# Kernel optimization log

Measured on AMD Instinct MI355X. Metric: run time of the kernel, lower is better.

The kernel has to match this reference:

```python
import jax, jax.numpy as jnp
import numpy as np

N_NODES = 100000
N_EDGES = 3200000
OUT_FEATURES = 16


def setup_inputs() -> dict:
    key = jax.random.key(0)
    k1, k2 = jax.random.split(key)
    edge = jax.random.randint(k1, (2, N_EDGES), 0, N_NODES, dtype=jnp.int64 if jax.config.jax_enable_x64 else jnp.int32)
    edge_w = jax.random.normal(k2, (N_EDGES, OUT_FEATURES), dtype=jnp.float32)
    return {
        "edge": edge,
        "edge_w": edge_w,
        "N": N_NODES,
        "E": N_EDGES,
        "out_features": OUT_FEATURES,
    }


def reference(edge, edge_w, N, E, out_features):
    # torch.sparse.sum over dim=1 of a [N, N, F] COO tensor == segment-sum of
    # edge_w grouped by the source index edge[0], producing dense [N, F].
    src = edge[0]  # [E]
    out = jax.ops.segment_sum(edge_w, src, num_segments=N)  # [N, F]
    return out
```

## Files before the change

### kernel.cpp

```cpp
#include <hip/hip_runtime.h>
#include <hip/hip_cooperative_groups.h>
#include <math.h>

namespace cg = cooperative_groups;


#define F 16
#define NPB 1024
#define NPB_SHIFT 10
#define MAXB 128
#define SCALE 256.0f
#define INV_SCALE (1.0f / 256.0f)

#define NBIN 256
#define BINT 512
#define NSPLIT 8
#define SLICES (NBIN / NSPLIT)
#define ACCT 512

#define FB 1024
#define FT 512
#define NBIN2 1024
#define NSPLIT2 8
#define SLICES2 (NBIN2 / NSPLIT2)

__device__ __forceinline__ unsigned long long qpack(float4 v) {
    long long q0 = (long long)__float2int_rn(v.x * SCALE);
    long long q1 = (long long)__float2int_rn(v.y * SCALE);
    long long q2 = (long long)__float2int_rn(v.z * SCALE);
    long long q3 = (long long)__float2int_rn(v.w * SCALE);
    return (unsigned long long)((q3 << 48) + (q2 << 32) + (q1 << 16) + q0);
}

__global__ __launch_bounds__(FT, 8) void spmm_fused(
    const int* __restrict__ src,
    const float* __restrict__ w,
    unsigned int* __restrict__ idbuf,
    unsigned int* __restrict__ cnt,
    unsigned long long* __restrict__ pbuf,
    float* __restrict__ out,
    int E, int B, int capb, int per_block, int N)
{
    __shared__ unsigned long long acc[NPB * 4];
    __shared__ unsigned int pos[MAXB];
    __shared__ unsigned int ksh[SLICES2];

    cg::grid_group grid = cg::this_grid();
    const int tid = threadIdx.x;
    const int bid = blockIdx.x;
    const int n4  = N * 4;
    unsigned long long* spill = pbuf + (size_t)NSPLIT2 * (size_t)n4;

    for (int i = tid; i < B; i += FT) pos[i] = 0;
    __syncthreads();

    const int lo = bid * per_block;
    const int hi = min(E, lo + per_block);
    for (int e = lo + tid * 2; e < hi; e += FT * 2) {
        int sa, sb = -1;
        if (e + 1 < hi) { int2 s2 = *(const int2*)(src + e); sa = s2.x; sb = s2.y; }
        else            { sa = src[e]; }
        {
            const int bk = sa >> NPB_SHIFT;
            const unsigned int off = (unsigned int)(sa & (NPB - 1));
            const unsigned int r = atomicAdd(&pos[bk], 1u);
            if (r < (unsigned int)capb) {
                idbuf[((size_t)bid * B + bk) * capb + r] = (off << 22) | (unsigned int)e;
            } else {
                const float4* wr = (const float4*)(w + (size_t)e * F);
                #pragma unroll
                for (int qq = 0; qq < 4; ++qq)
                    atomicAdd(&spill[(size_t)sa * 4 + qq], qpack(wr[qq]));
            }
        }
        if (sb >= 0) {
            const int e1 = e + 1;
            const int bk = sb >> NPB_SHIFT;
            const unsigned int off = (unsigned int)(sb & (NPB - 1));
            const unsigned int r = atomicAdd(&pos[bk], 1u);
            if (r < (unsigned int)capb) {
                idbuf[((size_t)bid * B + bk) * capb + r] = (off << 22) | (unsigned int)e1;
            } else {
                const float4* wr = (const float4*)(w + (size_t)e1 * F);
                #pragma unroll
                for (int qq = 0; qq < 4; ++qq)
                    atomicAdd(&spill[(size_t)sb * 4 + qq], qpack(wr[qq]));
            }
        }
    }
    __syncthreads();
    for (int i = tid; i < B; i += FT)
        cnt[bid * B + i] = min(pos[i], (unsigned int)capb);

    __threadfence();
    grid.sync();

    const int q   = tid & 3;
    const int st  = tid >> 2;
    const int sg  = st >> 4;
    const int s16 = st & 15;

    for (int t = bid; t < B * NSPLIT2; t += FB) {
        const int b  = t >> 3;
        const int sp = t & 7;

        for (int i = tid; i < NPB * 4; i += FT) acc[i] = 0ULL;
        if (tid < SLICES2) ksh[tid] = cnt[(sp * SLICES2 + tid) * B + b];
        __syncthreads();

        for (int sr = 0; sr < 16; ++sr) {
            const int s   = sr * 8 + sg;
            const int blk = sp * SLICES2 + s;
            const unsigned int k = ksh[s];
            const unsigned int* cell = idbuf + ((size_t)blk * B + b) * capb;
            #pragma unroll
            for (int tr = 0; tr < 4; ++tr) {
                const unsigned int slot = (unsigned int)(tr * 16 + s16);
                if (slot < k) {
                    const unsigned int entry = cell[slot];
                    const unsigned int off = entry >> 22;
                    const unsigned int e   = entry & 0x3FFFFFu;
                    const float4 v = *(const float4*)(w + (size_t)e * F + q * 4);
                    atomicAdd(&acc[off * 4 + q], qpack(v));
                }
            }
        }
        {
            const int s = st;
            const unsigned int k = ksh[s];
            if (k > 64u) {
                const int blk = sp * SLICES2 + s;
                const unsigned int* cell = idbuf + ((size_t)blk * B + b) * capb;
                for (unsigned int i = 64u; i < k; ++i) {
                    const unsigned int entry = cell[i];
                    const unsigned int off = entry >> 22;
                    const unsigned int e   = entry & 0x3FFFFFu;
                    const float4 v = *(const float4*)(w + (size_t)e * F + q * 4);
                    atomicAdd(&acc[off * 4 + q], qpack(v));
                }
            }
        }
        __syncthreads();

        const int nbase = b << NPB_SHIFT;
        const int lim = min(NPB, N - nbase);
        unsigned long long* dst = pbuf + (size_t)sp * n4 + (size_t)nbase * 4;
        for (int i = tid; i < lim * 4; i += FT) dst[i] = acc[i];
        __syncthreads();
    }

    __threadfence();
    grid.sync();

    for (int idx = bid * FT + tid; idx < n4; idx += FB * FT) {
        unsigned long long a = 0;
        #pragma unroll
        for (int s = 0; s < NSPLIT2 + 1; ++s) a += pbuf[(size_t)s * n4 + idx];
        long long tt = (long long)a;
        const int s0 = (int)(short)(tt & 0xffff);  tt = (tt - s0) >> 16;
        const int s1 = (int)(short)(tt & 0xffff);  tt = (tt - s1) >> 16;
        const int s2 = (int)(short)(tt & 0xffff);  tt = (tt - s2) >> 16;
        const int s3 = (int)(short)(tt & 0xffff);
        float4 o;
        o.x = (float)s0 * INV_SCALE;
        o.y = (float)s1 * INV_SCALE;
        o.z = (float)s2 * INV_SCALE;
        o.w = (float)s3 * INV_SCALE;
        ((float4*)out)[idx] = o;
    }
}

__global__ __launch_bounds__(BINT) void spmm_bin_id(
    const int* __restrict__ src,
    const float* __restrict__ w,
    unsigned int* __restrict__ idbuf,
    unsigned int* __restrict__ cnt,
    unsigned long long* __restrict__ spill,
    int E, int B, int capb, int per_block)
{
    __shared__ unsigned int pos[MAXB];
    const int tid = threadIdx.x;
    for (int i = tid; i < B; i += BINT) pos[i] = 0;
    __syncthreads();

    const int lo = blockIdx.x * per_block;
    const int hi = min(E, lo + per_block);

    for (int e = lo + tid; e < hi; e += BINT) {
        const int s = src[e];
        const int bk = s >> NPB_SHIFT;
        const unsigned int off = (unsigned int)(s & (NPB - 1));
        const unsigned int r = atomicAdd(&pos[bk], 1u);
        if (r < (unsigned int)capb) {
            idbuf[((size_t)blockIdx.x * B + bk) * capb + r] =
                (off << 22) | (unsigned int)e;
        } else {
            const float4* wr = (const float4*)(w + (size_t)e * F);
            #pragma unroll
            for (int q = 0; q < 4; ++q)
                atomicAdd(&spill[(size_t)s * 4 + q], qpack(wr[q]));
        }
    }
    __syncthreads();
    for (int i = tid; i < B; i += BINT)
        cnt[blockIdx.x * B + i] = min(pos[i], (unsigned int)capb);
}

__global__ __launch_bounds__(ACCT) void spmm_acc_g(
    const float* __restrict__ w,
    const unsigned int* __restrict__ idbuf,
    const unsigned int* __restrict__ cnt,
    unsigned long long* __restrict__ pbuf,
    int B, int capb, int N)
{
    __shared__ unsigned long long acc[NPB * 4];
    const int tid = threadIdx.x;
    const int b  = blockIdx.x >> 3;
    const int sp = blockIdx.x & 7;

    for (int i = tid; i < NPB * 4; i += ACCT) acc[i] = 0ULL;
    __syncthreads();

    const int q  = tid & 3;
    const int ei = tid >> 2;

    for (int sl = 0; sl < SLICES; ++sl) {
        const int blk = sp * SLICES + sl;
        const unsigned int k = cnt[blk * B + b];
        const unsigned int* base = idbuf + ((size_t)blk * B + b) * capb;
        for (unsigned int i = ei; i < k; i += ACCT / 4) {
            const unsigned int entry = base[i];
            const unsigned int off = entry >> 22;
            const unsigned int e   = entry & 0x3FFFFFu;
            const float4 v = *(const float4*)(w + (size_t)e * F + q * 4);
            atomicAdd(&acc[off * 4 + q], qpack(v));
        }
    }
    __syncthreads();

    const int nbase = b << NPB_SHIFT;
    const int lim = min(NPB, N - nbase);
    unsigned long long* dst = pbuf + (size_t)sp * ((size_t)N * 4) + (size_t)nbase * 4;
    for (int i = tid; i < lim * 4; i += ACCT) dst[i] = acc[i];
}

__global__ __launch_bounds__(256) void spmm_decode9(
    const unsigned long long* __restrict__ pbuf,
    float* __restrict__ out, int n4)
{
    const int idx = blockIdx.x * 256 + threadIdx.x;
    if (idx >= n4) return;
    unsigned long long a = 0;
    #pragma unroll
    for (int s = 0; s < NSPLIT + 1; ++s) a += pbuf[(size_t)s * n4 + idx];

    long long t = (long long)a;
    const int s0 = (int)(short)(t & 0xffff);  t = (t - s0) >> 16;
    const int s1 = (int)(short)(t & 0xffff);  t = (t - s1) >> 16;
    const int s2 = (int)(short)(t & 0xffff);  t = (t - s2) >> 16;
    const int s3 = (int)(short)(t & 0xffff);

    float4 o;
    o.x = (float)s0 * INV_SCALE;
    o.y = (float)s1 * INV_SCALE;
    o.z = (float)s2 * INV_SCALE;
    o.w = (float)s3 * INV_SCALE;
    ((float4*)out)[idx] = o;
}

__global__ __launch_bounds__(256) void spmm_scatter_gs(
    const int* __restrict__ src,
    const float* __restrict__ w,
    unsigned long long* __restrict__ ws,
    int total)
{
    const int stride = gridDim.x * blockDim.x;
    for (int idx = blockIdx.x * blockDim.x + threadIdx.x; idx < total; idx += stride) {
        const int e = idx >> 2, lane = idx & 3;
        const float4 v = ((const float4*)w)[idx];
        atomicAdd(&ws[src[e] * 4 + lane], qpack(v));
    }
}

__global__ __launch_bounds__(256) void spmm_decode1(
    const unsigned long long* __restrict__ ws,
    float* __restrict__ out, int n4)
{
    const int idx = blockIdx.x * 256 + threadIdx.x;
    if (idx >= n4) return;
    long long t = (long long)ws[idx];
    const int s0 = (int)(short)(t & 0xffff);  t = (t - s0) >> 16;
    const int s1 = (int)(short)(t & 0xffff);  t = (t - s1) >> 16;
    const int s2 = (int)(short)(t & 0xffff);  t = (t - s2) >> 16;
    const int s3 = (int)(short)(t & 0xffff);
    float4 o;
    o.x = (float)s0 * INV_SCALE;
    o.y = (float)s1 * INV_SCALE;
    o.z = (float)s2 * INV_SCALE;
    o.w = (float)s3 * INV_SCALE;
    ((float4*)out)[idx] = o;
}

extern "C" void kernel_launch(void* const* d_in, const int* in_sizes, int n_in,
                              void* d_out, int out_size, void* d_ws, size_t ws_size,
                              hipStream_t stream) {
    const int* edge = (const int*)d_in[0];
    const float* ew = (const float*)d_in[1];
    const int E = in_sizes[0] / 2;
    const int N = out_size / F;
    const int n4 = N * 4;
    float* out = (float*)d_out;

    const int B = (N + NPB - 1) >> NPB_SHIFT;

    static int coop_state = -1;
    if (coop_state < 0) {
        int maxb = 0, cus = 0;
        hipDeviceProp_t prop;
        int dev = 0;
        hipError_t e1 = hipGetDevice(&dev);
        hipError_t e2 = hipGetDeviceProperties(&prop, dev);
        if (e2 == hipSuccess) cus = prop.multiProcessorCount;
        hipError_t e3 = hipOccupancyMaxActiveBlocksPerMultiprocessor(
            &maxb, spmm_fused, FT, 0);
        coop_state = (e1 == hipSuccess && e3 == hipSuccess &&
                      (long)maxb * (long)cus >= FB) ? 1 : 0;
    }

    const double mean2 = (double)E / ((double)NBIN2 * (double)B);
    const double sig2  = sqrt(mean2 > 1.0 ? mean2 : 1.0);
    int capb2 = (int)(mean2 + 6.0 * sig2 + 8.0);
    capb2 = (capb2 + 15) & ~15;
    const size_t cnt2_b  = (size_t)NBIN2 * B * 4;
    const size_t pbuf2_b = (size_t)(NSPLIT2 + 1) * n4 * 8;
    const size_t fixed2  = ((cnt2_b + 255) & ~(size_t)255) + pbuf2_b + 512;
    if (ws_size > fixed2) {
        const size_t idroom = ws_size - fixed2;
        int capb2_max = (int)(idroom / ((size_t)NBIN2 * B * 4));
        capb2_max &= ~15;
        if (capb2 > capb2_max) capb2 = capb2_max;
    }
    const int capb2_min = ((int)(mean2 + 3.0 * sig2) + 15) & ~15;
    const size_t idbuf2_b = (size_t)NBIN2 * B * capb2 * 4;
    size_t off_cnt2  = (idbuf2_b + 255) & ~(size_t)255;
    size_t off_pbuf2 = (off_cnt2 + cnt2_b + 255) & ~(size_t)255;
    const size_t need2 = off_pbuf2 + pbuf2_b;

    const double mean = (double)E / ((double)NBIN * (double)B);
    int capb = (int)(mean + 8.0 * sqrt(mean > 1.0 ? mean : 1.0) + 16.0);
    capb = (capb + 15) & ~15;
    const size_t idbuf_b = (size_t)NBIN * B * capb * 4;
    size_t off_cnt  = (idbuf_b + 255) & ~(size_t)255;
    const size_t cnt_b = (size_t)NBIN * B * 4;
    size_t off_pbuf = (off_cnt + cnt_b + 255) & ~(size_t)255;
    const size_t pbuf_b = (size_t)(NSPLIT + 1) * n4 * 8;
    const size_t need = off_pbuf + pbuf_b;

    const int block = 256;
    const bool shape_ok = (B <= MAXB) && (E > 0) && (E < (1 << 22));

    if (shape_ok && coop_state == 1 && capb2 >= capb2_min && capb2 >= 16 &&
        need2 <= ws_size) {
        unsigned int* idbuf = (unsigned int*)d_ws;
        unsigned int* cnt   = (unsigned int*)((char*)d_ws + off_cnt2);
        unsigned long long* pbuf = (unsigned long long*)((char*)d_ws + off_pbuf2);
        unsigned long long* spill = pbuf + (size_t)NSPLIT2 * n4;

        hipMemsetAsync(spill, 0, (size_t)n4 * 8, stream);

        int per_block2 = (E + FB - 1) / FB;
        per_block2 = (per_block2 + 1) & ~1;

        int E_ = E, B_ = B, N_ = N, cap_ = capb2, pb_ = per_block2;
        void* kargs[] = { (void*)&edge, (void*)&ew, (void*)&idbuf, (void*)&cnt,
                          (void*)&pbuf, (void*)&out,
                          (void*)&E_, (void*)&B_, (void*)&cap_, (void*)&pb_, (void*)&N_ };
        hipError_t lr = hipLaunchCooperativeKernel(
            spmm_fused, dim3(FB), dim3(FT), kargs, 0, stream);
        if (lr == hipSuccess) return;
        coop_state = 0;
    }

    if (shape_ok && need <= ws_size) {
        unsigned int* idbuf = (unsigned int*)d_ws;
        unsigned int* cnt   = (unsigned int*)((char*)d_ws + off_cnt);
        unsigned long long* pbuf  = (unsigned long long*)((char*)d_ws + off_pbuf);
        unsigned long long* spill = pbuf + (size_t)NSPLIT * n4;

        hipMemsetAsync(spill, 0, (size_t)n4 * 8, stream);

        const int per_block = (E + NBIN - 1) / NBIN;
        spmm_bin_id<<<NBIN, BINT, 0, stream>>>(edge, ew, idbuf, cnt, spill,
                                               E, B, capb, per_block);
        spmm_acc_g<<<B * NSPLIT, ACCT, 0, stream>>>(ew, idbuf, cnt, pbuf,
                                                    B, capb, N);
        spmm_decode9<<<(n4 + block - 1) / block, block, 0, stream>>>(pbuf, out, n4);
    } else {
        unsigned long long* ws = (unsigned long long*)d_ws;
        hipMemsetAsync(ws, 0, (size_t)n4 * 8, stream);
        spmm_scatter_gs<<<2048, block, 0, stream>>>(edge, ew, ws, E * 4);
        spmm_decode1<<<(n4 + block - 1) / block, block, 0, stream>>>(ws, out, n4);
    }
}
```

Baseline: 355.2 us.

## Stage quantized edge payloads in bins instead of edge ids to avoid gather

The binning phase now reads each edge's 16 weights once, quantizes them, and writes the 32-byte packed payload plus a 16-bit node offset into the bin slot, instead of writing a packed (offset, edge id) word. The accumulate phase then streams these payloads contiguously with one lane per slot, and the shared accumulator moves to a feature-major layout, rather than gathering weight rows by edge id. This removes the random gather of the weight array in phase two. In exchange it adds much more workspace traffic (34 bytes per slot versus 4), lowers the occupancy hint in launch bounds, and shrinks the capacity cap, which may push more edges onto the global atomic spill path.

```diff
diff --git a/kernel.cpp b/kernel.cpp
--- a/kernel.cpp
+++ b/kernel.cpp
@@ -32,10 +32,11 @@
     return (unsigned long long)((q3 << 48) + (q2 << 32) + (q1 << 16) + q0);
 }
 
-__global__ __launch_bounds__(FT, 8) void spmm_fused(
+__global__ __launch_bounds__(FT, 4) void spmm_fused(
     const int* __restrict__ src,
     const float* __restrict__ w,
-    unsigned int* __restrict__ idbuf,
+    unsigned long long* __restrict__ pay,
+    unsigned short* __restrict__ off16,
     unsigned int* __restrict__ cnt,
     unsigned long long* __restrict__ pbuf,
     float* __restrict__ out,
@@ -56,37 +57,40 @@
 
     const int lo = bid * per_block;
     const int hi = min(E, lo + per_block);
-    for (int e = lo + tid * 2; e < hi; e += FT * 2) {
+    for (int e0 = lo + tid * 2; e0 < hi; e0 += FT * 2) {
         int sa, sb = -1;
-        if (e + 1 < hi) { int2 s2 = *(const int2*)(src + e); sa = s2.x; sb = s2.y; }
-        else            { sa = src[e]; }
-        {
-            const int bk = sa >> NPB_SHIFT;
-            const unsigned int off = (unsigned int)(sa & (NPB - 1));
+        if (e0 + 1 < hi) { int2 s2 = *(const int2*)(src + e0); sa = s2.x; sb = s2.y; }
+        else             { sa = src[e0]; }
+        #pragma unroll
+        for (int u = 0; u < 2; ++u) {
+            const int s = (u == 0) ? sa : sb;
+            if (s < 0 && u == 1) break;
+            const int e = e0 + u;
+            const float4* wr = (const float4*)(w + (size_t)e * F);
+            const float4 w0 = wr[0], w1 = wr[1], w2 = wr[2], w3 = wr[3];
+            const unsigned long long q0 = qpack(w0);
+            const unsigned long long q1 = qpack(w1);
+            const unsigned long long q2 = qpack(w2);
+            const unsigned long long q3 = qpack(w3);
+
+            const int bk = s >> NPB_SHIFT;
+            const unsigned int off = (unsigned int)(s & (NPB - 1));
             const unsigned int r = atomicAdd(&pos[bk], 1u);
             if (r < (unsigned int)capb) {
-                idbuf[((size_t)bid * B + bk) * capb + r] = (off << 22) | (unsigned int)e;
+                const size_t slot = ((size_t)bid * B + bk) * capb + r;
+                ulonglong2* ps = (ulonglong2*)(pay + slot * 4);
+                ulonglong2 p0; p0.x = q0; p0.y = q1;
+                ulonglong2 p1; p1.x = q2; p1.y = q3;
+                ps[0] = p0;
+                ps[1] = p1;
+                off16[slot] = (unsigned short)off;
             } else {
-                const float4* wr = (const float4*)(w + (size_t)e * F);
-                #pragma unroll
-                for (int qq = 0; qq < 4; ++qq)
-                    atomicAdd(&spill[(size_t)sa * 4 + qq], qpack(wr[qq]));
+                atomicAdd(&spill[(size_t)s * 4 + 0], q0);
+                atomicAdd(&spill[(size_t)s * 4 + 1], q1);
+                atomicAdd(&spill[(size_t)s * 4 + 2], q2);
+                atomicAdd(&spill[(size_t)s * 4 + 3], q3);
             }
         }
-        if (sb >= 0) {
-            const int e1 = e + 1;
-            const int bk = sb >> NPB_SHIFT;
-            const unsigned int off = (unsigned int)(sb & (NPB - 1));
-            const unsigned int r = atomicAdd(&pos[bk], 1u);
-            if (r < (unsigned int)capb) {
-                idbuf[((size_t)bid * B + bk) * capb + r] = (off << 22) | (unsigned int)e1;
-            } else {
-                const float4* wr = (const float4*)(w + (size_t)e1 * F);
-                #pragma unroll
-                for (int qq = 0; qq < 4; ++qq)
-                    atomicAdd(&spill[(size_t)sb * 4 + qq], qpack(wr[qq]));
-            }
-        }
     }
     __syncthreads();
     for (int i = tid; i < B; i += FT)
@@ -95,10 +99,8 @@
     __threadfence();
     grid.sync();
 
-    const int q   = tid & 3;
-    const int st  = tid >> 2;
-    const int sg  = st >> 4;
-    const int s16 = st & 15;
+    const int wv = tid >> 6;
+    const int ln = tid & 63;
 
     for (int t = bid; t < B * NSPLIT2; t += FB) {
         const int b  = t >> 3;
@@ -108,36 +110,19 @@
         if (tid < SLICES2) ksh[tid] = cnt[(sp * SLICES2 + tid) * B + b];
         __syncthreads();
 
-        for (int sr = 0; sr < 16; ++sr) {
-            const int s   = sr * 8 + sg;
-            const int blk = sp * SLICES2 + s;
+        for (int s = wv; s < SLICES2; s += 8) {
             const unsigned int k = ksh[s];
-            const unsigned int* cell = idbuf + ((size_t)blk * B + b) * capb;
-            #pragma unroll
-            for (int tr = 0; tr < 4; ++tr) {
-                const unsigned int slot = (unsigned int)(tr * 16 + s16);
-                if (slot < k) {
-                    const unsigned int entry = cell[slot];
-                    const unsigned int off = entry >> 22;
-                    const unsigned int e   = entry & 0x3FFFFFu;
-                    const float4 v = *(const float4*)(w + (size_t)e * F + q * 4);
-                    atomicAdd(&acc[off * 4 + q], qpack(v));
-                }
-            }
-        }
-        {
-            const int s = st;
-            const unsigned int k = ksh[s];
-            if (k > 64u) {
-                const int blk = sp * SLICES2 + s;
-                const unsigned int* cell = idbuf + ((size_t)blk * B + b) * capb;
-                for (unsigned int i = 64u; i < k; ++i) {
-                    const unsigned int entry = cell[i];
-                    const unsigned int off = entry >> 22;
-                    const unsigned int e   = entry & 0x3FFFFFu;
-                    const float4 v = *(const float4*)(w + (size_t)e * F + q * 4);
-                    atomicAdd(&acc[off * 4 + q], qpack(v));
-                }
+            const size_t cell = (size_t)(sp * SLICES2 + s) * B + b;
+            const ulonglong2* pp = (const ulonglong2*)(pay + cell * capb * 4);
+            const unsigned short* oo = off16 + cell * capb;
+            for (unsigned int slot = (unsigned int)ln; slot < k; slot += 64u) {
+                const ulonglong2 p0 = pp[slot * 2 + 0];
+                const ulonglong2 p1 = pp[slot * 2 + 1];
+                const unsigned int off = oo[slot];
+                atomicAdd(&acc[0 * NPB + off], p0.x);
+                atomicAdd(&acc[1 * NPB + off], p0.y);
+                atomicAdd(&acc[2 * NPB + off], p1.x);
+                atomicAdd(&acc[3 * NPB + off], p1.y);
             }
         }
         __syncthreads();
@@ -145,7 +130,8 @@
         const int nbase = b << NPB_SHIFT;
         const int lim = min(NPB, N - nbase);
         unsigned long long* dst = pbuf + (size_t)sp * n4 + (size_t)nbase * 4;
-        for (int i = tid; i < lim * 4; i += FT) dst[i] = acc[i];
+        for (int i = tid; i < lim * 4; i += FT)
+            dst[i] = acc[(i & 3) * NPB + (i >> 2)];
         __syncthreads();
     }
 
@@ -331,18 +317,21 @@
     const double sig2  = sqrt(mean2 > 1.0 ? mean2 : 1.0);
     int capb2 = (int)(mean2 + 6.0 * sig2 + 8.0);
     capb2 = (capb2 + 15) & ~15;
-    const size_t cnt2_b  = (size_t)NBIN2 * B * 4;
+    const size_t cells   = (size_t)NBIN2 * B;
+    const size_t cnt2_b  = cells * 4;
     const size_t pbuf2_b = (size_t)(NSPLIT2 + 1) * n4 * 8;
-    const size_t fixed2  = ((cnt2_b + 255) & ~(size_t)255) + pbuf2_b + 512;
+    const size_t fixed2  = ((cnt2_b + 255) & ~(size_t)255) + pbuf2_b + 1024;
     if (ws_size > fixed2) {
-        const size_t idroom = ws_size - fixed2;
-        int capb2_max = (int)(idroom / ((size_t)NBIN2 * B * 4));
+        const size_t room = ws_size - fixed2;
+        int capb2_max = (int)(room / (cells * 34));
         capb2_max &= ~15;
         if (capb2 > capb2_max) capb2 = capb2_max;
     }
     const int capb2_min = ((int)(mean2 + 3.0 * sig2) + 15) & ~15;
-    const size_t idbuf2_b = (size_t)NBIN2 * B * capb2 * 4;
-    size_t off_cnt2  = (idbuf2_b + 255) & ~(size_t)255;
+    const size_t pay_b   = cells * (size_t)capb2 * 32;
+    size_t off_off16 = (pay_b + 255) & ~(size_t)255;
+    const size_t off16_b = cells * (size_t)capb2 * 2;
+    size_t off_cnt2  = (off_off16 + off16_b + 255) & ~(size_t)255;
     size_t off_pbuf2 = (off_cnt2 + cnt2_b + 255) & ~(size_t)255;
     const size_t need2 = off_pbuf2 + pbuf2_b;
 
@@ -361,8 +350,9 @@
 
     if (shape_ok && coop_state == 1 && capb2 >= capb2_min && capb2 >= 16 &&
         need2 <= ws_size) {
-        unsigned int* idbuf = (unsigned int*)d_ws;
-        unsigned int* cnt   = (unsigned int*)((char*)d_ws + off_cnt2);
+        unsigned long long* pay = (unsigned long long*)d_ws;
+        unsigned short* off16   = (unsigned short*)((char*)d_ws + off_off16);
+        unsigned int* cnt       = (unsigned int*)((char*)d_ws + off_cnt2);
         unsigned long long* pbuf = (unsigned long long*)((char*)d_ws + off_pbuf2);
         unsigned long long* spill = pbuf + (size_t)NSPLIT2 * n4;
 
@@ -372,8 +362,8 @@
         per_block2 = (per_block2 + 1) & ~1;
 
         int E_ = E, B_ = B, N_ = N, cap_ = capb2, pb_ = per_block2;
-        void* kargs[] = { (void*)&edge, (void*)&ew, (void*)&idbuf, (void*)&cnt,
-                          (void*)&pbuf, (void*)&out,
+        void* kargs[] = { (void*)&edge, (void*)&ew, (void*)&pay, (void*)&off16,
+                          (void*)&cnt, (void*)&pbuf, (void*)&out,
                           (void*)&E_, (void*)&B_, (void*)&cap_, (void*)&pb_, (void*)&N_ };
         hipError_t lr = hipLaunchCooperativeKernel(
             spmm_fused, dim3(FB), dim3(FT), kargs, 0, stream);
```

Result: no change. 355.5 us (+0.1%).
